# Performance work log

Hardware: AMD Instinct MI355X
Metric: run time of the kernel (lower is better)

Reference implementation:

```python
import jax, jax.numpy as jnp
import numpy as np

H, ND, RD, VD = 16, 128, 64, 128  # heads, nope/rope/v head dims
EPS = 1e-6


def rmsnorm(x, g):
    return x * jax.lax.rsqrt(jnp.mean(x * x, axis=-1, keepdims=True) + EPS) * g


def apply_rope(x, cos, sin):
    # x: [B,T,h,D]; cos/sin: [1,T,1,D/2]; interleaved pair rotation
    x1, x2 = x[..., 0::2], x[..., 1::2]
    o1 = x1 * cos - x2 * sin
    o2 = x1 * sin + x2 * cos
    return jnp.stack([o1, o2], axis=-1).reshape(x.shape)


def setup_inputs() -> dict:
    key = jax.random.key(0)
    ks = jax.random.split(key, 10)
    B, T, D = 2, 2048, 2048
    QR, KVR = 1536, 512
    s = 0.02
    return {
        "x": jax.random.normal(ks[0], (B, T, D), jnp.float32),
        "w_cq": jax.random.normal(ks[1], (D, QR), jnp.float32) * s,
        "g_q": jnp.ones((QR,), jnp.float32),
        "w_ckv": jax.random.normal(ks[2], (D, KVR), jnp.float32) * s,
        "g_kv": jnp.ones((KVR,), jnp.float32),
        "w_dq_nope": jax.random.normal(ks[3], (QR, H * ND), jnp.float32) * s,
        "w_dq_rope": jax.random.normal(ks[4], (QR, H * RD), jnp.float32) * s,
        "w_dk_nope": jax.random.normal(ks[5], (KVR, H * ND), jnp.float32) * s,
        "w_dv": jax.random.normal(ks[6], (KVR, H * VD), jnp.float32) * s,
        "w_k_rope": jax.random.normal(ks[7], (D, RD), jnp.float32) * s,
        "w_out": jax.random.normal(ks[8], (H * VD, D), jnp.float32) * s,
    }


def reference(x, w_cq, g_q, w_ckv, g_kv, w_dq_nope, w_dq_rope,
              w_dk_nope, w_dv, w_k_rope, w_out):
    B, T, D = x.shape
    # low-rank latents + RMSNorm
    q_lat = rmsnorm(x @ w_cq, g_q)          # [B,T,QR]
    kv_lat = rmsnorm(x @ w_ckv, g_kv)        # [B,T,KVR]
    q_nope = (q_lat @ w_dq_nope).reshape(B, T, H, ND)
    q_rope = (q_lat @ w_dq_rope).reshape(B, T, H, RD)
    k_nope = (kv_lat @ w_dk_nope).reshape(B, T, H, ND)
    v = (kv_lat @ w_dv).reshape(B, T, H, VD)
    k_rope = (x @ w_k_rope).reshape(B, T, 1, RD)  # shared across heads
    # RoPE (start_pos = 0, no past_kv)
    pos = jnp.arange(T, dtype=jnp.float32)
    inv_freq = 1.0 / (10000.0 ** (jnp.arange(0, RD, 2, dtype=jnp.float32) / RD))
    ang = pos[:, None] * inv_freq[None, :]               # [T, RD/2]
    cos = jnp.cos(ang)[None, :, None, :]
    sin = jnp.sin(ang)[None, :, None, :]
    q_rope = apply_rope(q_rope, cos, sin)
    k_rope = apply_rope(k_rope, cos, sin)
    k_rope = jnp.broadcast_to(k_rope, (B, T, H, RD))
    q = jnp.concatenate([q_nope, q_rope], axis=-1).transpose(0, 2, 1, 3)  # [B,H,T,ND+RD]
    k = jnp.concatenate([k_nope, k_rope], axis=-1).transpose(0, 2, 1, 3)
    v_t = v.transpose(0, 2, 1, 3)                                        # [B,H,T,VD]
    # causal SDPA, scale = 1/sqrt(head_dim)
    scale = 1.0 / jnp.sqrt(jnp.asarray(ND + RD, jnp.float32))
    scores = jnp.einsum('bhqd,bhkd->bhqk', q, k) * scale
    causal = jnp.tril(jnp.ones((T, T), dtype=bool))
    scores = jnp.where(causal[None, None], scores, -jnp.inf)
    attn = jax.nn.softmax(scores, axis=-1)
    out = jnp.einsum('bhqk,bhkd->bhqd', attn, v_t)
    out = out.transpose(0, 2, 1, 3).reshape(B, T, H * VD) @ w_out        # [B,T,D]
    return out, k, v_t
```

## Files before the change

### kernel.cpp

```cpp
#include <hip/hip_runtime.h>
#include <cstdint>
#include <cstddef>

typedef _Float16 HT;
typedef _Float16 h8 __attribute__((ext_vector_type(8)));
typedef _Float16 h4 __attribute__((ext_vector_type(4)));
typedef float f32x4 __attribute__((ext_vector_type(4)));

constexpr int Tn  = 2048;
constexpr int Dm  = 2048;
constexpr int Hh  = 16;
constexpr int RDc = 64;
constexpr int QRc = 1536;
constexpr int KVRc= 512;
constexpr int BT  = 4096;

#define VWAIT(N) asm volatile("s_waitcnt vmcnt(" #N ")" ::: "memory")
#define SBAR()   __builtin_amdgcn_s_barrier()

__device__ __forceinline__ f32x4 mfma16(h8 a, h8 b, f32x4 c) {
    return __builtin_amdgcn_mfma_f32_16x16x32_f16(a, b, c, 0, 0, 0);
}
__device__ __forceinline__ void gload_lds16(const void* g, void* l) {
    __builtin_amdgcn_global_load_lds(
        (const __attribute__((address_space(1))) unsigned int*)g,
        (__attribute__((address_space(3))) unsigned int*)l, 16, 0, 0);
}

__global__ __launch_bounds__(256)
void cstab_kernel(float2* __restrict__ cs)
{
    const int idx = blockIdx.x * 256 + threadIdx.x;
    const int t = idx >> 5, i = idx & 31;
    const float ang = (float)t * exp2f(-(float)i * (13.287712379549449f / 32.f));
    cs[idx] = make_float2(cosf(ang), sinf(ang));
}

struct WT8 {
    const float* s[8];
    HT* d[8];
    int K[8], N[8], start[8];
};

__global__ __launch_bounds__(256)
void wtrans8_kernel(WT8 p)
{
    __shared__ float Ts[64][65];
    int seg = 0;
    #pragma unroll
    for (int i = 1; i < 8; i++) if ((int)blockIdx.x >= p.start[i]) seg = i;
    const float* src = p.s[seg];
    HT* dst = p.d[seg];
    const int K = p.K[seg], N = p.N[seg];
    const int bx = blockIdx.x - p.start[seg];
    const int nx = N >> 6;
    const int n0 = (bx % nx) * 64, k0 = (bx / nx) * 64;
    const int tid = threadIdx.x;
    {
        const int r = tid >> 2, c0 = (tid & 3) * 16;
        const float* s = src + (size_t)(k0 + r) * N + n0 + c0;
        #pragma unroll
        for (int j = 0; j < 4; j++)
            *reinterpret_cast<f32x4*>(&Ts[r][c0 + j * 4]) = *reinterpret_cast<const f32x4*>(s + j * 4);
    }
    __syncthreads();
    {
        const int c = tid >> 2, kq = (tid & 3) * 16;
        h8 o0, o1;
        #pragma unroll
        for (int j = 0; j < 8; j++) { o0[j] = (HT)Ts[kq + j][c]; o1[j] = (HT)Ts[kq + 8 + j][c]; }
        HT* d = dst + (size_t)(n0 + c) * K + k0 + kq;
        *reinterpret_cast<h8*>(d)     = o0;
        *reinterpret_cast<h8*>(d + 8) = o1;
    }
}

__global__ __launch_bounds__(256)
void convx_kernel(const float* __restrict__ x, HT* __restrict__ x16)
{
    const size_t i = ((size_t)blockIdx.x * 256 + threadIdx.x) * 8;
    f32x4 a = *reinterpret_cast<const f32x4*>(x + i);
    f32x4 b = *reinterpret_cast<const f32x4*>(x + i + 4);
    h8 v;
    #pragma unroll
    for (int j = 0; j < 4; j++) { v[j] = (HT)a[j]; v[4 + j] = (HT)b[j]; }
    *reinterpret_cast<h8*>(x16 + i) = v;
}

template<int EPI>
__global__ __launch_bounds__(256)
void gemm16d(const HT* __restrict__ A, const HT* __restrict__ Bt, const int K,
             HT* __restrict__ o1, HT* __restrict__ o2, HT* __restrict__ o3,
             float* __restrict__ f1, float* __restrict__ f2,
             const float2* __restrict__ cstab)
{
    __shared__ HT As[2][4096];
    __shared__ HT Bs[2][4096];

    const int tid  = threadIdx.x;
    const int lane = tid & 63;
    const int l15  = lane & 15, l4 = lane >> 4;
    const int w    = tid >> 6;
    const int wr   = w >> 1, wc = w & 1;
    const int m0   = blockIdx.y * 128;
    const int n0   = blockIdx.x * 128;

    f32x4 acc[4][4] = {};
    const int nk = K >> 5;

    const int schunk = ((lane & 3) ^ ((lane >> 2) & 3) ^ ((lane >> 4) & 3)) * 8;

#define GSTAGE(as_, bs_, kt_) do {                                             \
    _Pragma("unroll")                                                          \
    for (int i_ = 0; i_ < 2; i_++) {                                           \
        const int row_ = (w * 2 + i_) * 16 + (lane >> 2);                      \
        gload_lds16(A  + (size_t)(m0 + row_) * K + (kt_) + schunk,             \
                    (as_) + (w * 2 + i_) * 512);                               \
        gload_lds16(Bt + (size_t)(n0 + row_) * K + (kt_) + schunk,             \
                    (bs_) + (w * 2 + i_) * 512);                               \
    } } while (0)

    GSTAGE(As[0], Bs[0], 0);

    const int sl = (l4 ^ (l15 & 3) ^ ((l15 >> 2) & 3)) * 8;

    for (int kt = 0; kt < nk; kt++) {
        HT* as = As[kt & 1];
        HT* bs = Bs[kt & 1];
        if (kt + 1 < nk) {
            GSTAGE(As[(kt + 1) & 1], Bs[(kt + 1) & 1], (kt + 1) * 32);
            VWAIT(4);
        } else {
            VWAIT(0);
        }
        SBAR();

        h8 af[4], bf[4];
        #pragma unroll
        for (int f = 0; f < 4; f++)
            af[f] = *reinterpret_cast<const h8*>(&as[(wr * 64 + f * 16 + l15) * 32 + sl]);
        #pragma unroll
        for (int g = 0; g < 4; g++)
            bf[g] = *reinterpret_cast<const h8*>(&bs[(wc * 64 + g * 16 + l15) * 32 + sl]);
        #pragma unroll
        for (int f = 0; f < 4; f++)
            #pragma unroll
            for (int g = 0; g < 4; g++)
                acc[f][g] = mfma16(af[f], bf[g], acc[f][g]);
        SBAR();
    }
#undef GSTAGE

    #pragma unroll
    for (int f = 0; f < 4; f++) {
        #pragma unroll
        for (int g = 0; g < 4; g++) {
            const int row = m0 + wr * 64 + f * 16 + l4 * 4;
            const int col = n0 + wc * 64 + g * 16 + l15;
            if constexpr (EPI == 3) {
                #pragma unroll
                for (int r = 0; r < 4; r++)
                    f1[(size_t)(row + r) * 2048 + col] = acc[f][g][r];
            } else if constexpr (EPI == 0) {
                if (col < 1536) {
                    #pragma unroll
                    for (int r = 0; r < 4; r++)
                        o1[(size_t)(row + r) * 1536 + col] = (HT)acc[f][g][r];
                } else if (col < 2048) {
                    #pragma unroll
                    for (int r = 0; r < 4; r++)
                        o2[(size_t)(row + r) * 512 + (col - 1536)] = (HT)acc[f][g][r];
                } else if (col < 2112) {
                    const int cc = col - 2048;
                    const int i = cc >> 1;
                    const bool odd = cc & 1;
                    #pragma unroll
                    for (int r = 0; r < 4; r++) {
                        const int t = (row + r) & (Tn - 1);
                        const float2 cs = cstab[t * 32 + i];
                        const float v = acc[f][g][r];
                        const float p = __shfl_xor(v, 1);
                        const float ov = odd ? p * cs.y + v * cs.x : v * cs.x - p * cs.y;
                        o3[(size_t)(row + r) * 64 + cc] = (HT)ov;
                    }
                }
            } else if constexpr (EPI == 1) {
                if (col < 2048) {
                    #pragma unroll
                    for (int r = 0; r < 4; r++)
                        o1[(size_t)(row + r) * 2048 + col] = (HT)acc[f][g][r];
                } else {
                    const int cc = col - 2048;
                    const int i = (cc & 63) >> 1;
                    const bool odd = cc & 1;
                    #pragma unroll
                    for (int r = 0; r < 4; r++) {
                        const int t = (row + r) & (Tn - 1);
                        const float2 cs = cstab[t * 32 + i];
                        const float v = acc[f][g][r];
                        const float p = __shfl_xor(v, 1);
                        const float ov = odd ? p * cs.y + v * cs.x : v * cs.x - p * cs.y;
                        o2[(size_t)(row + r) * 1024 + cc] = (HT)ov;
                    }
                }
            } else {
                if (col < 2048) {
                    const int h = col >> 7, d = col & 127;
                    #pragma unroll
                    for (int r = 0; r < 4; r++) {
                        const int rw = row + r;
                        const int b = rw >> 11, t = rw & (Tn - 1);
                        o1[(size_t)rw * 2048 + col] = (HT)acc[f][g][r];
                        f1[((size_t)(b * Hh + h) * Tn + t) * 192 + d] = acc[f][g][r];
                    }
                } else {
                    const int c2 = col - 2048;
                    const int h = c2 >> 7, d = c2 & 127;
                    const int b = row >> 11, t0 = row & (Tn - 1);
                    h4 pk;
                    #pragma unroll
                    for (int r = 0; r < 4; r++) {
                        f2[((size_t)(b * Hh + h) * Tn + t0 + r) * 128 + d] = acc[f][g][r];
                        pk[r] = (HT)acc[f][g][r];
                    }
                    *reinterpret_cast<h4*>(&o3[((size_t)(b * Hh + h) * 128 + d) * Tn + t0]) = pk;
                }
            }
        }
    }
}

__global__ __launch_bounds__(256)
void kropebc_kernel(const HT* __restrict__ kr16, float* __restrict__ out_k)
{
    const int idx = blockIdx.x * 256 + threadIdx.x;
    const int j4 = (idx & 15) * 4;
    const int t  = (idx >> 4) & (Tn - 1);
    const int b  = idx >> 15;
    h4 v = *reinterpret_cast<const h4*>(&kr16[((size_t)(b * Tn + t)) * 64 + j4]);
    f32x4 f;
    #pragma unroll
    for (int r = 0; r < 4; r++) f[r] = (float)v[r];
    #pragma unroll
    for (int h = 0; h < Hh; h++)
        *reinterpret_cast<f32x4*>(&out_k[((size_t)(b * Hh + h) * Tn + t) * 192 + 128 + j4]) = f;
}

__global__ __launch_bounds__(256)
void rmsnorm2_kernel(HT* __restrict__ Xa, const float* __restrict__ ga,
                     HT* __restrict__ Xb, const float* __restrict__ gb)
{
    const int which = blockIdx.y;
    HT* X = which ? Xb : Xa;
    const float* g = which ? gb : ga;
    const int N = which ? 512 : 1536;
    const int row = blockIdx.x;
    HT* x = X + (size_t)row * N;
    float ss = 0.f;
    for (int i = threadIdx.x * 8; i < N; i += 2048) {
        h8 v = *reinterpret_cast<const h8*>(&x[i]);
        #pragma unroll
        for (int j = 0; j < 8; j++) { float f = (float)v[j]; ss += f * f; }
    }
    #pragma unroll
    for (int sh = 32; sh >= 1; sh >>= 1) ss += __shfl_xor(ss, sh);
    __shared__ float red[4];
    if ((threadIdx.x & 63) == 0) red[threadIdx.x >> 6] = ss;
    __syncthreads();
    const float tot = red[0] + red[1] + red[2] + red[3];
    const float scale = rsqrtf(tot / (float)N + 1e-6f);
    for (int i = threadIdx.x * 8; i < N; i += 2048) {
        h8 v = *reinterpret_cast<const h8*>(&x[i]);
        f32x4 g0 = *reinterpret_cast<const f32x4*>(&g[i]);
        f32x4 g1 = *reinterpret_cast<const f32x4*>(&g[i + 4]);
        #pragma unroll
        for (int j = 0; j < 4; j++) { v[j]   = (HT)((float)v[j]   * scale * g0[j]);
                                      v[4+j] = (HT)((float)v[4+j] * scale * g1[j]); }
        *reinterpret_cast<h8*>(&x[i]) = v;
    }
}

__global__ __launch_bounds__(256, 2)
void attn9_kernel(const HT* __restrict__ qn, const HT* __restrict__ qr,
                  const HT* __restrict__ kn, const HT* __restrict__ kr16,
                  const HT* __restrict__ vt, HT* __restrict__ ao)
{
    __shared__ HT Ks_n[64 * 128];
    __shared__ HT Vs[128 * 64];
    __shared__ HT Ps[4][32][72];

    const int tid  = threadIdx.x;
    const int lane = tid & 63;
    const int l15  = lane & 15, l4 = lane >> 4;
    const int w    = tid >> 6;

    const int bid = blockIdx.x;
    const int j   = bid >> 5;
    const int h   = bid & 15;
    const int b   = (bid >> 4) & 1;
    const int thi = 31 - j;

    const size_t bT = (size_t)b * Tn;
    const HT* vt_h = vt + ((size_t)(b * Hh + h) * 128) * Tn;
    const HT* krb  = kr16 + bT * 64;

    const int qw0 = j   * 64 + w * 16;
    const int qw1 = thi * 64 + w * 16;

    h8 aq0[6], aq1[6];
    {
        const HT sc = (HT)(0.07216878364870323f * 1.4426950408889634f);
        const size_t rq0 = bT + qw0 + l15;
        const HT* pn = qn + rq0 * 2048 + h * 128 + l4 * 8;
        #pragma unroll
        for (int f = 0; f < 4; f++) aq0[f] = *reinterpret_cast<const h8*>(pn + f * 32) * sc;
        const HT* pr = qr + rq0 * 1024 + h * 64 + l4 * 8;
        aq0[4] = *reinterpret_cast<const h8*>(pr) * sc;
        aq0[5] = *reinterpret_cast<const h8*>(pr + 32) * sc;
        const size_t rq1 = bT + qw1 + l15;
        const HT* pn1 = qn + rq1 * 2048 + h * 128 + l4 * 8;
        #pragma unroll
        for (int f = 0; f < 4; f++) aq1[f] = *reinterpret_cast<const h8*>(pn1 + f * 32) * sc;
        const HT* pr1 = qr + rq1 * 1024 + h * 64 + l4 * 8;
        aq1[4] = *reinterpret_cast<const h8*>(pr1) * sc;
        aq1[5] = *reinterpret_cast<const h8*>(pr1 + 32) * sc;
    }

    f32x4 o0[8] = {}, o1[8] = {};
    float m0v[4] = {-1e30f, -1e30f, -1e30f, -1e30f};
    float m1v[4] = {-1e30f, -1e30f, -1e30f, -1e30f};
    float l0v[4] = {0.f, 0.f, 0.f, 0.f};
    float l1v[4] = {0.f, 0.f, 0.f, 0.f};

#define SMX(sv, mv, lv, ov, qwx, prow)                                          \
{                                                                               \
    float a_[4][4]; float mxr_[4]; bool ok_ = true;                             \
    _Pragma("unroll")                                                           \
    for (int r = 0; r < 4; r++) {                                               \
        const int qrow = (qwx) + l4 * 4 + r;                                    \
        _Pragma("unroll")                                                       \
        for (int c = 0; c < 4; c++)                                             \
            a_[r][c] = (kb + c * 16 + l15 <= qrow) ? sv[c][r] : -1e30f;         \
        mxr_[r] = fmaxf(fmaxf(a_[r][0], a_[r][1]), fmaxf(a_[r][2], a_[r][3]));  \
        ok_ = ok_ && (mxr_[r] <= mv[r] + 8.f);                                  \
    }                                                                           \
    if (__builtin_expect((bool)__all(ok_), 1)) {                                \
        _Pragma("unroll")                                                       \
        for (int r = 0; r < 4; r++) {                                           \
            float rs = 0.f;                                                     \
            _Pragma("unroll")                                                   \
            for (int c = 0; c < 4; c++) {                                       \
                const float e = __builtin_exp2f(a_[r][c] - mv[r]);              \
                rs += e;                                                        \
                Ps[w][(prow) + l4 * 4 + r][c * 16 + l15] = (HT)e;               \
            }                                                                   \
            lv[r] += rs;                                                        \
        }                                                                       \
    } else {                                                                    \
        float al_[4];                                                           \
        _Pragma("unroll")                                                       \
        for (int r = 0; r < 4; r++) {                                           \
            float mx = mxr_[r];                                                 \
            _Pragma("unroll")                                                   \
            for (int sh = 1; sh < 16; sh <<= 1) mx = fmaxf(mx, __shfl_xor(mx, sh)); \
            const float mn = fmaxf(mv[r], mx);                                  \
            al_[r] = __builtin_exp2f(mv[r] - mn);                               \
            mv[r] = mn;                                                         \
            float rs = 0.f;                                                     \
            _Pragma("unroll")                                                   \
            for (int c = 0; c < 4; c++) {                                       \
                const float e = __builtin_exp2f(a_[r][c] - mn);                 \
                rs += e;                                                        \
                Ps[w][(prow) + l4 * 4 + r][c * 16 + l15] = (HT)e;               \
            }                                                                   \
            lv[r] = lv[r] * al_[r] + rs;                                        \
        }                                                                       \
        _Pragma("unroll")                                                       \
        for (int g = 0; g < 8; g++)                                             \
            _Pragma("unroll")                                                   \
            for (int r = 0; r < 4; r++) ov[g][r] *= al_[r];                     \
    }                                                                           \
}

#define KBODY(ACT0)                                                             \
{                                                                               \
    f32x4 s0[4] = {}, s1[4] = {};                                               \
    __builtin_amdgcn_s_setprio(1);                                              \
    _Pragma("unroll")                                                           \
    for (int c = 0; c < 4; c++) {                                               \
        const int kr = c * 16 + l15;                                            \
        const HT* rp = krb + (size_t)(kb + kr) * 64 + l4 * 8;                   \
        const h8 br0 = *reinterpret_cast<const h8*>(rp);                        \
        const h8 br1 = *reinterpret_cast<const h8*>(rp + 32);                   \
        const int sw = (kr & 7) << 4;                                           \
        const char* kbase = (const char*)Ks_n + kr * 256;                       \
        _Pragma("unroll")                                                       \
        for (int f = 0; f < 4; f++) {                                           \
            const h8 kf = *(const h8*)(kbase + ((f * 64 + l4 * 16) ^ sw));      \
            s1[c] = mfma16(aq1[f], kf, s1[c]);                                  \
            if (ACT0) s0[c] = mfma16(aq0[f], kf, s0[c]);                        \
        }                                                                       \
        s1[c] = mfma16(aq1[4], br0, s1[c]);                                     \
        s1[c] = mfma16(aq1[5], br1, s1[c]);                                     \
        if (ACT0) { s0[c] = mfma16(aq0[4], br0, s0[c]);                         \
                    s0[c] = mfma16(aq0[5], br1, s0[c]); }                       \
    }                                                                           \
    __builtin_amdgcn_s_setprio(0);                                              \
    SMX(s1, m1v, l1v, o1, qw1, 16);                                             \
    if (ACT0) SMX(s0, m0v, l0v, o0, qw0, 0);                                    \
    const h8 ap10 = *reinterpret_cast<const h8*>(&Ps[w][16 + l15][l4 * 8]);     \
    const h8 ap11 = *reinterpret_cast<const h8*>(&Ps[w][16 + l15][32 + l4 * 8]);\
    h8 ap00 = ap10, ap01 = ap11;                                                \
    if (ACT0) {                                                                 \
        ap00 = *reinterpret_cast<const h8*>(&Ps[w][l15][l4 * 8]);               \
        ap01 = *reinterpret_cast<const h8*>(&Ps[w][l15][32 + l4 * 8]);          \
    }                                                                           \
    __builtin_amdgcn_s_setprio(1);                                              \
    _Pragma("unroll")                                                           \
    for (int g = 0; g < 8; g++) {                                               \
        const int d = g * 16 + l15;                                             \
        const int sw = (d & 7) << 4;                                            \
        const char* vbase = (const char*)Vs + d * 128;                          \
        const h8 v0 = *(const h8*)(vbase + ((l4 * 16) ^ sw));                   \
        const h8 v1 = *(const h8*)(vbase + ((64 + l4 * 16) ^ sw));              \
        o1[g] = mfma16(ap10, v0, o1[g]);                                        \
        o1[g] = mfma16(ap11, v1, o1[g]);                                        \
        if (ACT0) { o0[g] = mfma16(ap00, v0, o0[g]);                            \
                    o0[g] = mfma16(ap01, v1, o0[g]); }                          \
    }                                                                           \
    __builtin_amdgcn_s_setprio(0);                                              \
}

    const int nkb = thi + 1;
    for (int kb64 = 0; kb64 < nkb; kb64++) {
        const int kb = kb64 * 64;
        __syncthreads();
        #pragma unroll
        for (int jj = 0; jj < 4; jj++) {
            const int r = (w * 4 + jj) * 4 + l4;
            const int cl = (l15 & 8) | ((l15 & 7) ^ (r & 7));
            gload_lds16(kn + (bT + kb + r) * 2048 + h * 128 + cl * 8,
                        &Ks_n[(w * 4 + jj) * 512]);
        }
        #pragma unroll
        for (int jj = 0; jj < 4; jj++) {
            const int d = (w * 4 + jj) * 8 + (lane >> 3);
            const int cl = (lane & 7) ^ (d & 7);
            gload_lds16(vt_h + (size_t)d * Tn + kb + cl * 8,
                        &Vs[(w * 4 + jj) * 512]);
        }
        __syncthreads();

        if (kb <= qw0 + 15) KBODY(1) else KBODY(0)
    }
#undef KBODY
#undef SMX

    {
        const size_t orow = bT + qw1 + l4 * 4;
        #pragma unroll
        for (int r = 0; r < 4; r++) {
            float rsum = l1v[r];
            #pragma unroll
            for (int sh = 1; sh < 16; sh <<= 1) rsum += __shfl_xor(rsum, sh);
            const float inv = 1.0f / rsum;
            HT* dst = ao + (orow + r) * 2048 + h * 128 + l15;
            #pragma unroll
            for (int g = 0; g < 8; g++) dst[g * 16] = (HT)(o1[g][r] * inv);
        }
    }
    {
        const size_t orow = bT + qw0 + l4 * 4;
        #pragma unroll
        for (int r = 0; r < 4; r++) {
            float rsum = l0v[r];
            #pragma unroll
            for (int sh = 1; sh < 16; sh <<= 1) rsum += __shfl_xor(rsum, sh);
            const float inv = 1.0f / rsum;
            HT* dst = ao + (orow + r) * 2048 + h * 128 + l15;
            #pragma unroll
            for (int g = 0; g < 8; g++) dst[g * 16] = (HT)(o0[g][r] * inv);
        }
    }
}

extern "C" void kernel_launch(void* const* d_in, const int* in_sizes, int n_in,
                              void* d_out, int out_size, void* d_ws, size_t ws_size,
                              hipStream_t stream)
{
    const float* x     = (const float*)d_in[0];
    const float* w_cq  = (const float*)d_in[1];
    const float* g_q   = (const float*)d_in[2];
    const float* w_ckv = (const float*)d_in[3];
    const float* g_kv  = (const float*)d_in[4];
    const float* w_dqn = (const float*)d_in[5];
    const float* w_dqr = (const float*)d_in[6];
    const float* w_dkn = (const float*)d_in[7];
    const float* w_dv  = (const float*)d_in[8];
    const float* w_kr  = (const float*)d_in[9];
    const float* w_out = (const float*)d_in[10];

    char* ws = (char*)d_ws;
    HT* cqT   = (HT*)(ws + 0);
    HT* ckvT  = (HT*)(ws + 6291456);
    HT* krT   = (HT*)(ws + 8388608);
    HT* dqnT  = (HT*)(ws + 8912896);
    HT* dqrT  = (HT*)(ws + 15204352);
    HT* dknT  = (HT*)(ws + 18350080);
    HT* dvT   = (HT*)(ws + 20447232);
    HT* outT  = (HT*)(ws + 22544384);
    HT* cq    = (HT*)(ws + 30932992);
    HT* ckv   = (HT*)(ws + 43515904);
    HT* qn    = (HT*)(ws + 47710208);
    HT* qr    = (HT*)(ws + 64487424);
    HT* kn    = (HT*)(ws + 72876032);
    HT* kr16  = (HT*)(ws + 89653248);
    HT* vt    = (HT*)(ws + 0);
    HT* x16   = qn;
    HT* ao    = qn;

    float* out_o = (float*)d_out;
    float* out_k = out_o + (size_t)BT * Dm;
    float* out_v = out_k + (size_t)2 * Hh * Tn * 192;
    float2* cstab = (float2*)out_v;

    const dim3 blk(256);

    cstab_kernel<<<dim3(256), blk, 0, stream>>>(cstab);

    WT8 wt;
    wt.s[0]=w_cq;  wt.d[0]=cqT;  wt.K[0]=2048; wt.N[0]=1536;
    wt.s[1]=w_ckv; wt.d[1]=ckvT; wt.K[1]=2048; wt.N[1]=512;
    wt.s[2]=w_kr;  wt.d[2]=krT;  wt.K[2]=2048; wt.N[2]=64;
    wt.s[3]=w_dqn; wt.d[3]=dqnT; wt.K[3]=1536; wt.N[3]=2048;
    wt.s[4]=w_dqr; wt.d[4]=dqrT; wt.K[4]=1536; wt.N[4]=1024;
    wt.s[5]=w_dkn; wt.d[5]=dknT; wt.K[5]=512;  wt.N[5]=2048;
    wt.s[6]=w_dv;  wt.d[6]=dvT;  wt.K[6]=512;  wt.N[6]=2048;
    wt.s[7]=w_out; wt.d[7]=outT; wt.K[7]=2048; wt.N[7]=2048;
    {
        int acc = 0;
        for (int i = 0; i < 8; i++) {
            wt.start[i] = acc;
            acc += (wt.N[i] >> 6) * (wt.K[i] >> 6);
        }
        wtrans8_kernel<<<dim3(acc), blk, 0, stream>>>(wt);
    }

    convx_kernel<<<dim3(4096), blk, 0, stream>>>(x, x16);

    gemm16d<0><<<dim3(17, BT/128), blk, 0, stream>>>(x16, cqT, Dm,
        cq, ckv, kr16, nullptr, nullptr, cstab);
    kropebc_kernel<<<dim3(256), blk, 0, stream>>>(kr16, out_k);

    rmsnorm2_kernel<<<dim3(BT, 2), blk, 0, stream>>>(cq, g_q, ckv, g_kv);

    gemm16d<1><<<dim3(24, BT/128), blk, 0, stream>>>(cq, dqnT, QRc,
        qn, qr, nullptr, nullptr, nullptr, cstab);
    gemm16d<2><<<dim3(32, BT/128), blk, 0, stream>>>(ckv, dknT, KVRc,
        kn, nullptr, vt, out_k, out_v, nullptr);

    attn9_kernel<<<dim3(512), blk, 0, stream>>>(qn, qr, kn, kr16, vt, ao);

    gemm16d<3><<<dim3(16, BT/128), blk, 0, stream>>>(ao, outT, Dm,
        nullptr, nullptr, nullptr, out_o, nullptr, nullptr);
}
```

Baseline: 346.9 us.

## Double-buffer attention K/V tiles with 32-key blocks and stage rope keys in LDS

The attention kernel now processes 32-key blocks instead of 64 and keeps two LDS buffers, so the next tile's K-nope, K-rope and V loads are issued before computing on the current one, synchronised with vmcnt waits and raw barriers. The shared rope keys, previously read straight from global memory inside the inner loop, are now staged into swizzled LDS as well. Wave-level skipping of fully masked tiles is added for the second query block. Smaller tiles double the number of barriers and softmax rescale steps per row.

```diff
diff --git a/kernel.cpp b/kernel.cpp
--- a/kernel.cpp
+++ b/kernel.cpp
@@ -281,13 +281,14 @@
 }
 
 __global__ __launch_bounds__(256, 2)
-void attn9_kernel(const HT* __restrict__ qn, const HT* __restrict__ qr,
-                  const HT* __restrict__ kn, const HT* __restrict__ kr16,
-                  const HT* __restrict__ vt, HT* __restrict__ ao)
-{
-    __shared__ HT Ks_n[64 * 128];
-    __shared__ HT Vs[128 * 64];
-    __shared__ HT Ps[4][32][72];
+void attn10_kernel(const HT* __restrict__ qn, const HT* __restrict__ qr,
+                   const HT* __restrict__ kn, const HT* __restrict__ kr16,
+                   const HT* __restrict__ vt, HT* __restrict__ ao)
+{
+    __shared__ HT Ks_n[2][32 * 128];
+    __shared__ HT Ks_r[2][32 * 64];
+    __shared__ HT Vs[2][128 * 32];
+    __shared__ HT Ps[4][32][40];
 
     const int tid  = threadIdx.x;
     const int lane = tid & 63;
@@ -302,7 +303,6 @@
 
     const size_t bT = (size_t)b * Tn;
     const HT* vt_h = vt + ((size_t)(b * Hh + h) * 128) * Tn;
-    const HT* krb  = kr16 + bT * 64;
 
     const int qw0 = j   * 64 + w * 16;
     const int qw1 = thi * 64 + w * 16;
@@ -332,16 +332,40 @@
     float l0v[4] = {0.f, 0.f, 0.f, 0.f};
     float l1v[4] = {0.f, 0.f, 0.f, 0.f};
 
+#define STAGE(sl_, kb_) do {                                                    \
+    _Pragma("unroll")                                                           \
+    for (int jj = 0; jj < 2; jj++) {                                            \
+        const int cc = w * 2 + jj;                                              \
+        const int r_ = cc * 4 + (lane >> 4);                                    \
+        const int cl = (l15 & 8) | ((l15 & 7) ^ (r_ & 7));                      \
+        gload_lds16(kn + (bT + (kb_) + r_) * 2048 + h * 128 + cl * 8,           \
+                    &Ks_n[sl_][cc * 512]);                                      \
+    }                                                                           \
+    {                                                                           \
+        const int r_ = w * 8 + (lane >> 3);                                     \
+        const int cl = (lane & 7) ^ (r_ & 7);                                   \
+        gload_lds16(kr16 + (bT + (kb_) + r_) * 64 + cl * 8,                     \
+                    &Ks_r[sl_][w * 512]);                                       \
+    }                                                                           \
+    _Pragma("unroll")                                                           \
+    for (int jj = 0; jj < 2; jj++) {                                            \
+        const int cc = w * 2 + jj;                                              \
+        const int d_ = cc * 16 + (lane >> 2);                                   \
+        const int cl = (lane & 3) ^ (d_ & 3);                                   \
+        gload_lds16(vt_h + (size_t)d_ * Tn + (kb_) + cl * 8,                    \
+                    &Vs[sl_][cc * 512]);                                        \
+    } } while (0)
+
 #define SMX(sv, mv, lv, ov, qwx, prow)                                          \
 {                                                                               \
-    float a_[4][4]; float mxr_[4]; bool ok_ = true;                             \
+    float a_[4][2]; float mxr_[4]; bool ok_ = true;                             \
     _Pragma("unroll")                                                           \
     for (int r = 0; r < 4; r++) {                                               \
         const int qrow = (qwx) + l4 * 4 + r;                                    \
         _Pragma("unroll")                                                       \
-        for (int c = 0; c < 4; c++)                                             \
+        for (int c = 0; c < 2; c++)                                             \
             a_[r][c] = (kb + c * 16 + l15 <= qrow) ? sv[c][r] : -1e30f;         \
-        mxr_[r] = fmaxf(fmaxf(a_[r][0], a_[r][1]), fmaxf(a_[r][2], a_[r][3]));  \
+        mxr_[r] = fmaxf(a_[r][0], a_[r][1]);                                    \
         ok_ = ok_ && (mxr_[r] <= mv[r] + 8.f);                                  \
     }                                                                           \
     if (__builtin_expect((bool)__all(ok_), 1)) {                                \
@@ -349,7 +373,7 @@
         for (int r = 0; r < 4; r++) {                                           \
             float rs = 0.f;                                                     \
             _Pragma("unroll")                                                   \
-            for (int c = 0; c < 4; c++) {                                       \
+            for (int c = 0; c < 2; c++) {                                       \
                 const float e = __builtin_exp2f(a_[r][c] - mv[r]);              \
                 rs += e;                                                        \
                 Ps[w][(prow) + l4 * 4 + r][c * 16 + l15] = (HT)e;               \
@@ -368,7 +392,7 @@
             mv[r] = mn;                                                         \
             float rs = 0.f;                                                     \
             _Pragma("unroll")                                                   \
-            for (int c = 0; c < 4; c++) {                                       \
+            for (int c = 0; c < 2; c++) {                                       \
                 const float e = __builtin_exp2f(a_[r][c] - mn);                 \
                 rs += e;                                                        \
                 Ps[w][(prow) + l4 * 4 + r][c * 16 + l15] = (HT)e;               \
@@ -384,16 +408,16 @@
 
 #define KBODY(ACT0)                                                             \
 {                                                                               \
-    f32x4 s0[4] = {}, s1[4] = {};                                               \
+    f32x4 s0[2] = {}, s1[2] = {};                                               \
     __builtin_amdgcn_s_setprio(1);                                              \
     _Pragma("unroll")                                                           \
-    for (int c = 0; c < 4; c++) {                                               \
+    for (int c = 0; c < 2; c++) {                                               \
         const int kr = c * 16 + l15;                                            \
-        const HT* rp = krb + (size_t)(kb + kr) * 64 + l4 * 8;                   \
-        const h8 br0 = *reinterpret_cast<const h8*>(rp);                        \
-        const h8 br1 = *reinterpret_cast<const h8*>(rp + 32);                   \
         const int sw = (kr & 7) << 4;                                           \
-        const char* kbase = (const char*)Ks_n + kr * 256;                       \
+        const char* kbase = (const char*)&Ks_n[sl][0] + kr * 256;               \
+        const char* rbase = (const char*)&Ks_r[sl][0] + kr * 128;               \
+        const h8 br0 = *(const h8*)(rbase + ((l4 * 16) ^ sw));                  \
+        const h8 br1 = *(const h8*)(rbase + ((64 + l4 * 16) ^ sw));             \
         _Pragma("unroll")                                                       \
         for (int f = 0; f < 4; f++) {                                           \
             const h8 kf = *(const h8*)(kbase + ((f * 64 + l4 * 16) ^ sw));      \
@@ -408,53 +432,42 @@
     __builtin_amdgcn_s_setprio(0);                                              \
     SMX(s1, m1v, l1v, o1, qw1, 16);                                             \
     if (ACT0) SMX(s0, m0v, l0v, o0, qw0, 0);                                    \
-    const h8 ap10 = *reinterpret_cast<const h8*>(&Ps[w][16 + l15][l4 * 8]);     \
-    const h8 ap11 = *reinterpret_cast<const h8*>(&Ps[w][16 + l15][32 + l4 * 8]);\
-    h8 ap00 = ap10, ap01 = ap11;                                                \
-    if (ACT0) {                                                                 \
-        ap00 = *reinterpret_cast<const h8*>(&Ps[w][l15][l4 * 8]);               \
-        ap01 = *reinterpret_cast<const h8*>(&Ps[w][l15][32 + l4 * 8]);          \
-    }                                                                           \
+    const h8 ap1 = *reinterpret_cast<const h8*>(&Ps[w][16 + l15][l4 * 8]);      \
+    h8 ap0 = ap1;                                                               \
+    if (ACT0) ap0 = *reinterpret_cast<const h8*>(&Ps[w][l15][l4 * 8]);          \
     __builtin_amdgcn_s_setprio(1);                                              \
     _Pragma("unroll")                                                           \
     for (int g = 0; g < 8; g++) {                                               \
         const int d = g * 16 + l15;                                             \
-        const int sw = (d & 7) << 4;                                            \
-        const char* vbase = (const char*)Vs + d * 128;                          \
-        const h8 v0 = *(const h8*)(vbase + ((l4 * 16) ^ sw));                   \
-        const h8 v1 = *(const h8*)(vbase + ((64 + l4 * 16) ^ sw));              \
-        o1[g] = mfma16(ap10, v0, o1[g]);                                        \
-        o1[g] = mfma16(ap11, v1, o1[g]);                                        \
-        if (ACT0) { o0[g] = mfma16(ap00, v0, o0[g]);                            \
-                    o0[g] = mfma16(ap01, v1, o0[g]); }                          \
+        const int swd = (d & 3) << 4;                                           \
+        const char* vbase = (const char*)&Vs[sl][0] + d * 64;                   \
+        const h8 v0 = *(const h8*)(vbase + ((l4 * 16) ^ swd));                  \
+        o1[g] = mfma16(ap1, v0, o1[g]);                                         \
+        if (ACT0) o0[g] = mfma16(ap0, v0, o0[g]);                               \
     }                                                                           \
     __builtin_amdgcn_s_setprio(0);                                              \
 }
 
-    const int nkb = thi + 1;
-    for (int kb64 = 0; kb64 < nkb; kb64++) {
-        const int kb = kb64 * 64;
-        __syncthreads();
-        #pragma unroll
-        for (int jj = 0; jj < 4; jj++) {
-            const int r = (w * 4 + jj) * 4 + l4;
-            const int cl = (l15 & 8) | ((l15 & 7) ^ (r & 7));
-            gload_lds16(kn + (bT + kb + r) * 2048 + h * 128 + cl * 8,
-                        &Ks_n[(w * 4 + jj) * 512]);
+    const int nkb = (thi + 1) * 2;
+    STAGE(0, 0);
+
+    for (int t = 0; t < nkb; t++) {
+        const int kb = t * 32;
+        const int sl = t & 1;
+        if (t + 1 < nkb) {
+            STAGE(sl ^ 1, kb + 32);
+            VWAIT(5);
+        } else {
+            VWAIT(0);
         }
-        #pragma unroll
-        for (int jj = 0; jj < 4; jj++) {
-            const int d = (w * 4 + jj) * 8 + (lane >> 3);
-            const int cl = (lane & 7) ^ (d & 7);
-            gload_lds16(vt_h + (size_t)d * Tn + kb + cl * 8,
-                        &Vs[(w * 4 + jj) * 512]);
-        }
-        __syncthreads();
-
-        if (kb <= qw0 + 15) KBODY(1) else KBODY(0)
+        SBAR();
+        if (kb <= qw0 + 15)      KBODY(1)
+        else if (kb <= qw1 + 15) KBODY(0)
+        SBAR();
     }
 #undef KBODY
 #undef SMX
+#undef STAGE
 
     {
         const size_t orow = bT + qw1 + l4 * 4;
@@ -559,7 +572,7 @@
     gemm16d<2><<<dim3(32, BT/128), blk, 0, stream>>>(ckv, dknT, KVRc,
         kn, nullptr, vt, out_k, out_v, nullptr);
 
-    attn9_kernel<<<dim3(512), blk, 0, stream>>>(qn, qr, kn, kr16, vt, ao);
+    attn10_kernel<<<dim3(512), blk, 0, stream>>>(qn, qr, kn, kr16, vt, ao);
 
     gemm16d<3><<<dim3(16, BT/128), blk, 0, stream>>>(ao, outT, Dm,
         nullptr, nullptr, nullptr, out_o, nullptr, nullptr);
```

New measurement: 340.8 us. About the same (-1.8%).
